# Performance work log

Measured on AMD Instinct MI355X. Metric: run time of the kernel, lower is better.

## Reference

```python
import jax, jax.numpy as jnp
import numpy as np

B, L, D = 2, 2048, 2048
H, KV = 32, 8
HD = D // H          # 64
REP = H // KV        # 4


def setup_inputs() -> dict:
    key = jax.random.key(0)
    ks = jax.random.split(key, 6)
    x = jax.random.normal(ks[0], (B, L, D), dtype=jnp.float32)
    # weights stored [in, out] (transpose of torch Linear weight), scaled for stability
    wq = jax.random.normal(ks[1], (D, H * HD), dtype=jnp.float32) * 0.02
    wk = jax.random.normal(ks[2], (D, KV * HD), dtype=jnp.float32) * 0.02
    wv = jax.random.normal(ks[3], (D, KV * HD), dtype=jnp.float32) * 0.02
    wo = jax.random.normal(ks[4], (H * HD, D), dtype=jnp.float32) * 0.02
    # RoPE frequencies: freqs_cis = exp(i * pos * theta), theta_j = 10000^{-2j/HD}
    inv_freq = 1.0 / (10000.0 ** (jnp.arange(0, HD, 2, dtype=jnp.float32) / HD))  # [HD/2]
    angles = jnp.arange(L, dtype=jnp.float32)[:, None] * inv_freq[None, :]        # [L, HD/2]
    freqs_cos = jnp.cos(angles)
    freqs_sin = jnp.sin(angles)
    # additive causal mask [L, L] (prefill from start_pos=0)
    mask = jnp.where(jnp.tril(jnp.ones((L, L), dtype=bool)), 0.0, -jnp.inf).astype(jnp.float32)
    return {"x": x, "start_pos": 0, "freqs_cos": freqs_cos, "freqs_sin": freqs_sin,
            "mask": mask, "wq": wq, "wk": wk, "wv": wv, "wo": wo}


def _apply_rope(t, cos, sin):
    # t: [B, L, h, HD]; cos/sin: [L, HD/2] -> broadcast [1, L, 1, HD/2]
    tp = t.reshape(*t.shape[:-1], HD // 2, 2)
    a, b = tp[..., 0], tp[..., 1]
    c = cos[None, :, None, :]
    s = sin[None, :, None, :]
    ra = a * c - b * s
    rb = a * s + b * c
    return jnp.stack([ra, rb], axis=-1).reshape(t.shape)


def reference(x, start_pos, freqs_cos, freqs_sin, mask, wq, wk, wv, wo):
    xq = jnp.einsum('bld,de->ble', x, wq).reshape(B, L, H, HD)
    xk = jnp.einsum('bld,de->ble', x, wk).reshape(B, L, KV, HD)
    xv = jnp.einsum('bld,de->ble', x, wv).reshape(B, L, KV, HD)
    xq = _apply_rope(xq, freqs_cos, freqs_sin)
    xk = _apply_rope(xk, freqs_cos, freqs_sin)
    # (cache write of xk/xv is a dead side effect in the torch module; omitted)
    # GQA: query head (g*REP + r) attends to kv head g  == repeat_interleave semantics
    q = xq.transpose(0, 2, 1, 3).reshape(B, KV, REP, L, HD)  # [B,KV,REP,L,HD]
    k = xk.transpose(0, 2, 1, 3)                              # [B,KV,L,HD]
    v = xv.transpose(0, 2, 1, 3)
    scale = 1.0 / jnp.sqrt(jnp.float32(HD))
    scores = jnp.einsum('bgrld,bgmd->bgrlm', q, k) * scale + mask  # [B,KV,REP,L,L]
    attn = jax.nn.softmax(scores, axis=-1)
    out = jnp.einsum('bgrlm,bgmd->bgrld', attn, v)            # [B,KV,REP,L,HD]
    out = out.reshape(B, H, L, HD).transpose(0, 2, 1, 3).reshape(B, L, H * HD)
    return jnp.einsum('ble,ed->bld', out, wo)
```

## Files before the change

kernel.cpp:

```cpp
#include <hip/hip_runtime.h>
#include <hip/hip_bf16.h>
#include <math.h>

typedef __bf16 bf16_t;
typedef __bf16 bf16x8 __attribute__((ext_vector_type(8)));
typedef __bf16 bf16x4 __attribute__((ext_vector_type(4)));
typedef __bf16 bf16x2 __attribute__((ext_vector_type(2)));
typedef float  f32x4  __attribute__((ext_vector_type(4)));
typedef int    i32x4  __attribute__((ext_vector_type(4)));

#define B_  2
#define L_  2048
#define D_  2048
#define H_  32
#define KV_ 8
#define HD_ 64

static __device__ __forceinline__ void gload_lds16(const bf16_t* g, void* l)
{
    __builtin_amdgcn_global_load_lds(
        (const __attribute__((address_space(1))) void*)g,
        (__attribute__((address_space(3))) void*)l, 16, 0, 0);
}

static __device__ __forceinline__ int packbf(float a, float b)
{
    bf16x2 t; t[0] = (bf16_t)a; t[1] = (bf16_t)b;
    return __builtin_bit_cast(int, t);
}

static __device__ __forceinline__ void pl32(int& a, int& b)
{
    asm("v_permlane32_swap_b32 %0, %1" : "+v"(a), "+v"(b));
}
static __device__ __forceinline__ void pl16(int& a, int& b)
{
    asm("v_permlane16_swap_b32 %0, %1" : "+v"(a), "+v"(b));
}

#define WAITV3() asm volatile("s_waitcnt vmcnt(3)" ::: "memory")
#define WAITV2() asm volatile("s_waitcnt vmcnt(2)" ::: "memory")
#define WAITV0() asm volatile("s_waitcnt vmcnt(0)" ::: "memory")
#define WAITL0() asm volatile("s_waitcnt lgkmcnt(0)" ::: "memory")

__global__ void prep_k(const float* __restrict__ wq, const float* __restrict__ wk,
                       const float* __restrict__ wv, const float* __restrict__ wo,
                       const float* __restrict__ xf,
                       bf16_t* __restrict__ Wqkv, bf16_t* __restrict__ WoT,
                       bf16_t* __restrict__ xb)
{
    __shared__ bf16_t tile[32][33];
    const int z  = blockIdx.z;
    const int tx = threadIdx.x, ty = threadIdx.y;

    if (z == 4) {
        const size_t base = ((size_t)(blockIdx.y * 64 + blockIdx.x) * 256
                             + ty * 32 + tx) * 8;
        const float4 v0 = *(const float4*)(xf + base);
        const float4 v1 = *(const float4*)(xf + base + 4);
        bf16x8 o;
        o[0] = (bf16_t)v0.x; o[1] = (bf16_t)v0.y; o[2] = (bf16_t)v0.z; o[3] = (bf16_t)v0.w;
        o[4] = (bf16_t)v1.x; o[5] = (bf16_t)v1.y; o[6] = (bf16_t)v1.z; o[7] = (bf16_t)v1.w;
        *(bf16x8*)(xb + base) = o;
        return;
    }

    const float* in; bf16_t* out; int C;
    if (z == 0)      { in = wq; out = Wqkv;                  C = 2048; }
    else if (z == 1) { in = wk; out = Wqkv + 2048ull * 2048; C = 512;  }
    else if (z == 2) { in = wv; out = Wqkv + 2560ull * 2048; C = 512;  }
    else             { in = wo; out = WoT;                   C = 2048; }

    const int bx = blockIdx.x * 32, by = blockIdx.y * 32;
    if (bx >= C) return;
    const int R = 2048;
#pragma unroll
    for (int i = ty; i < 32; i += 8)
        tile[i][tx] = (bf16_t)in[(size_t)(by + i) * C + bx + tx];
    __syncthreads();
#pragma unroll
    for (int i = ty; i < 32; i += 8)
        out[(size_t)(bx + i) * R + by + tx] = tile[tx][i];
}

template <typename InT>
__global__ void transpose_cast(const InT* __restrict__ in, bf16_t* __restrict__ out,
                               int R, int C)
{
    __shared__ bf16_t tile[32][33];
    const int bx = blockIdx.x * 32, by = blockIdx.y * 32;
    in  += (size_t)blockIdx.z * R * C;
    out += (size_t)blockIdx.z * R * C;
    const int tx = threadIdx.x, ty = threadIdx.y;
#pragma unroll
    for (int i = ty; i < 32; i += 8)
        tile[i][tx] = (bf16_t)(float)in[(size_t)(by + i) * C + bx + tx];
    __syncthreads();
#pragma unroll
    for (int i = ty; i < 32; i += 8)
        out[(size_t)(bx + i) * R + by + tx] = tile[tx][i];
}

#define FRAG(base, row, kk) \
    (*(const bf16x8*)((base) + (size_t)(row) * 128 + ((((kk) * 4 + quad) ^ sw8) << 4)))

#define STG_A(kt, h, buf) do {                                                        \
    gload_lds16(Ag + (size_t)((h) * 128)      * 2048 + (size_t)(kt) * 64,             \
                sdst + (buf) * 32768 + (h) * 16384);                                  \
    gload_lds16(Ag + (size_t)((h) * 128 + 64) * 2048 + (size_t)(kt) * 64,             \
                sdst + (buf) * 32768 + (h) * 16384 + 8192);                           \
} while (0)

#define STG_BU(kt, u, buf)                                                            \
    gload_lds16(Bg + (size_t)((u) * 64) * 2048 + (size_t)(kt) * 64,                   \
                sdst + 65536 + (buf) * 24576 + (u) * 8192)

#define QTILE(AB, BB, S1, S2, S3, S4, VMW)                                            \
  {                                  \
    _Pragma("unroll") for (int m = 0; m < 4; m++) {                                   \
        Afr[m][0] = FRAG(AB, arow + m * 16, 0);                                       \
        Afr[m][1] = FRAG(AB, arow + m * 16, 1); }                                     \
    _Pragma("unroll") for (int n = 0; n < 2; n++) {                                   \
        B01[n][0] = FRAG(BB, brow + n * 16, 0);                                       \
        B01[n][1] = FRAG(BB, brow + n * 16, 1); }                                     \
    S1;                                                                               \
    asm volatile("s_waitcnt lgkmcnt(8)" ::: "memory");                                \
    __builtin_amdgcn_s_barrier();                                                     \
    WAITL0();                                                                         \
    __builtin_amdgcn_s_setprio(1);                                                    \
    _Pragma("unroll") for (int m = 0; m < 4; m++)                                     \
      _Pragma("unroll") for (int n = 0; n < 2; n++)                                   \
        _Pragma("unroll") for (int kk = 0; kk < 2; kk++)                              \
          acc[m][n] = __builtin_amdgcn_mfma_f32_16x16x32_bf16(                        \
              Afr[m][kk], B01[n][kk], acc[m][n], 0, 0, 0);                            \
    __builtin_amdgcn_s_setprio(0);                                                    \
    __builtin_amdgcn_s_barrier();                                                     \
  }                                                                                   \
  {                                              \
    B2f[0] = FRAG(BB, brow + 32, 0);                                                  \
    B2f[1] = FRAG(BB, brow + 32, 1);                                                  \
    S2;                                                                               \
    __builtin_amdgcn_s_barrier();                                                     \
    WAITL0();                                                                         \
    __builtin_amdgcn_s_setprio(1);                                                    \
    _Pragma("unroll") for (int m = 0; m < 4; m++)                                     \
      _Pragma("unroll") for (int kk = 0; kk < 2; kk++)                                \
          acc[m][2] = __builtin_amdgcn_mfma_f32_16x16x32_bf16(                        \
              Afr[m][kk], B2f[kk], acc[m][2], 0, 0, 0);                               \
    __builtin_amdgcn_s_setprio(0);                                                    \
    __builtin_amdgcn_s_barrier();                                                     \
  }                                                                                   \
  {                                            \
    _Pragma("unroll") for (int m = 0; m < 4; m++) {                                   \
        Afr[m][0] = FRAG(AB, arow + (m + 4) * 16, 0);                                 \
        Afr[m][1] = FRAG(AB, arow + (m + 4) * 16, 1); }                               \
    S3;                                                                               \
    __builtin_amdgcn_s_barrier();                                                     \
    WAITL0();                                                                         \
    __builtin_amdgcn_s_setprio(1);                                                    \
    _Pragma("unroll") for (int m = 0; m < 4; m++)                                     \
      _Pragma("unroll") for (int kk = 0; kk < 2; kk++)                                \
          acc[m + 4][2] = __builtin_amdgcn_mfma_f32_16x16x32_bf16(                    \
              Afr[m][kk], B2f[kk], acc[m + 4][2], 0, 0, 0);                           \
    __builtin_amdgcn_s_setprio(0);                                                    \
    __builtin_amdgcn_s_barrier();                                                     \
  }                                                                                   \
  {                                \
    S4;                                                                               \
    VMW;                                                                              \
    __builtin_amdgcn_s_barrier();                                                     \
    __builtin_amdgcn_s_setprio(1);                                                    \
    _Pragma("unroll") for (int m = 0; m < 4; m++)                                     \
      _Pragma("unroll") for (int n = 0; n < 2; n++)                                   \
        _Pragma("unroll") for (int kk = 0; kk < 2; kk++)                              \
          acc[m + 4][n] = __builtin_amdgcn_mfma_f32_16x16x32_bf16(                    \
              Afr[m][kk], B01[n][kk], acc[m + 4][n], 0, 0, 0);                        \
    __builtin_amdgcn_s_setprio(0);                                                    \
    __builtin_amdgcn_s_barrier();                                                     \
  }

__global__ __launch_bounds__(512, 2) void gemm_qkv(
    const bf16_t* __restrict__ A,
    const bf16_t* __restrict__ BT,
    bf16_t* __restrict__ Qb, bf16_t* __restrict__ Kb, bf16_t* __restrict__ Vb)
{
    extern __shared__ __attribute__((aligned(16))) char DLDS[];
    constexpr int NITER = 2048 / 64 / 2;

    const int tid  = threadIdx.x;
    const int wave = tid >> 6;
    const int lane = tid & 63;
    const int quad = lane >> 4;
    const int l16  = lane & 15;
    const int wr   = wave >> 2;
    const int wc   = wave & 3;

    const int id   = blockIdx.x;
    const int w    = id >> 3;
    const int m0   = ((id & 7) * 2 + (w & 1)) * 256;
    const int n0   = (w >> 1) * 192;

    const int srow  = tid >> 3;
    const int swcol = ((tid & 7) ^ (srow & 7)) * 8;
    const bf16_t* Ag = A  + (size_t)(m0 + srow) * 2048 + swcol;
    const bf16_t* Bg = BT + (size_t)(n0 + srow) * 2048 + swcol;
    char* sdst = DLDS + tid * 16;

    const char* AB0 = DLDS;
    const char* AB1 = DLDS + 32768;
    const char* BB0 = DLDS + 65536;
    const char* BB1 = DLDS + 90112;
    const int sw8  = l16 & 7;
    const int arow = wr * 128 + l16;
    const int brow = wc * 48 + l16;

    f32x4 acc[8][3];
    const f32x4 zf = {0.f, 0.f, 0.f, 0.f};
#pragma unroll
    for (int i = 0; i < 8; i++)
#pragma unroll
        for (int j = 0; j < 3; j++) acc[i][j] = zf;

    bf16x8 Afr[4][2], B01[2][2], B2f[2];

    STG_BU(0, 0, 0); STG_BU(0, 1, 0); STG_BU(0, 2, 0);
    STG_A(0, 0, 0);  STG_A(0, 1, 0);
    STG_BU(1, 0, 1); STG_BU(1, 1, 1); STG_BU(1, 2, 1);
    WAITV3();
    __builtin_amdgcn_s_barrier();

    for (int i = 0; i < NITER; ++i) {
        const int t1 = 2 * i + 1;
        const int t2 = 2 * i + 2;
        const int t3 = 2 * i + 3;
        const bool more = (i + 1 < NITER);

        QTILE(AB0, BB0,
              STG_A(t1, 0, 1),
              STG_A(t1, 1, 1),
              if (more) { STG_BU(t2, 0, 0); STG_BU(t2, 1, 0); },
              if (more) { STG_BU(t2, 2, 0); },
              if (more) { WAITV3(); } else { WAITV0(); })
        QTILE(AB1, BB1,
              if (more) STG_A(t2, 0, 0),
              if (more) STG_A(t2, 1, 0),
              if (more) { STG_BU(t3, 0, 1); STG_BU(t3, 1, 1); },
              if (more) { STG_BU(t3, 2, 1); },
              if (more) { WAITV3(); } else { WAITV0(); })
    }

    const float cs = 0.18033688011112042f;
#pragma unroll
    for (int mt = 0; mt < 8; mt++)
#pragma unroll
        for (int nt = 0; nt < 3; nt++)
#pragma unroll
            for (int r = 0; r < 4; r++) {
                const int row  = m0 + wr * 128 + mt * 16 + quad * 4 + r;
                const int gcol = n0 + wc * 48 + nt * 16 + l16;
                const float v  = acc[mt][nt][r];
                if (gcol < 2048)
                    Qb[(size_t)row * 2048 + gcol] = (bf16_t)v;
                else if (gcol < 2560)
                    Kb[(size_t)row * 512 + (gcol - 2048)] = (bf16_t)(v * cs);
                else
                    Vb[(size_t)row * 512 + (gcol - 2560)] = (bf16_t)v;
            }
}

#undef FRAG
#undef STG_A
#undef STG_BU
#undef QTILE

#define OFRAG(base, row, kk) \
    (*(const bf16x8*)((base) + (size_t)(row) * 128 + ((((kk) * 4 + quad) ^ sw8) << 4)))

#define OSTG_A(kt, h, buf) do {                                                       \
    gload_lds16(Ag + (size_t)((h) * 128)      * 2048 + (size_t)(kt) * 64,             \
                adst + (buf) * 32768 + (h) * 16384);                                  \
    gload_lds16(Ag + (size_t)((h) * 128 + 64) * 2048 + (size_t)(kt) * 64,             \
                adst + (buf) * 32768 + (h) * 16384 + 8192);                           \
} while (0)

#define OSTG_B(kt, buf) do {                                                          \
    gload_lds16(Bg + (size_t)(kt) * 64,                       bdst + (buf) * 16384);  \
    gload_lds16(Bg + (size_t)64 * 2048 + (size_t)(kt) * 64,   bdst + (buf) * 16384 + 8192); \
} while (0)

#define OTILE(AB, BB, SA, SB, VMW)                                                    \
  {                                             \
    _Pragma("unroll") for (int m = 0; m < 4; m++) {                                   \
        Afr[m][0] = OFRAG(AB, arow + m * 16, 0);                                      \
        Afr[m][1] = OFRAG(AB, arow + m * 16, 1); }                                    \
    _Pragma("unroll") for (int n = 0; n < 2; n++) {                                   \
        Bfr[n][0] = OFRAG(BB, brow + n * 16, 0);                                      \
        Bfr[n][1] = OFRAG(BB, brow + n * 16, 1); }                                    \
    SA;                                                                               \
    asm volatile("s_waitcnt lgkmcnt(8)" ::: "memory");                                \
    __builtin_amdgcn_s_barrier();                                                     \
    WAITL0();                                                                         \
    __builtin_amdgcn_s_setprio(1);                                                    \
    _Pragma("unroll") for (int m = 0; m < 4; m++)                                     \
      _Pragma("unroll") for (int n = 0; n < 2; n++)                                   \
        _Pragma("unroll") for (int kk = 0; kk < 2; kk++)                              \
          acc[m][n] = __builtin_amdgcn_mfma_f32_16x16x32_bf16(                        \
              Afr[m][kk], Bfr[n][kk], acc[m][n], 0, 0, 0);                            \
    __builtin_amdgcn_s_setprio(0);                                                    \
    __builtin_amdgcn_s_barrier();                                                     \
  }                                                                                   \
  {                                \
    _Pragma("unroll") for (int m = 0; m < 4; m++) {                                   \
        Afr[m][0] = OFRAG(AB, arow + (m + 4) * 16, 0);                                \
        Afr[m][1] = OFRAG(AB, arow + (m + 4) * 16, 1); }                              \
    SB;                                                                               \
    VMW;                                                                              \
    __builtin_amdgcn_s_barrier();                                                     \
    WAITL0();                                                                         \
    __builtin_amdgcn_s_setprio(1);                                                    \
    _Pragma("unroll") for (int m = 0; m < 4; m++)                                     \
      _Pragma("unroll") for (int n = 0; n < 2; n++)                                   \
        _Pragma("unroll") for (int kk = 0; kk < 2; kk++)                              \
          acc[m + 4][n] = __builtin_amdgcn_mfma_f32_16x16x32_bf16(                    \
              Afr[m][kk], Bfr[n][kk], acc[m + 4][n], 0, 0, 0);                        \
    __builtin_amdgcn_s_setprio(0);                                                    \
    __builtin_amdgcn_s_barrier();                                                     \
  }

__global__ __launch_bounds__(512, 2) void gemm_out(
    const bf16_t* __restrict__ A,
    const bf16_t* __restrict__ BT,
    float* __restrict__ C)
{
    extern __shared__ __attribute__((aligned(16))) char DLDS[];
    constexpr int NITER = 2048 / 64 / 2;

    const int tid  = threadIdx.x;
    const int wave = tid >> 6;
    const int lane = tid & 63;
    const int quad = lane >> 4;
    const int l16  = lane & 15;
    const int wr   = wave >> 2;
    const int wc   = wave & 3;

    const int id   = blockIdx.x;
    const int w    = id >> 3;
    const int m0   = ((id & 7) * 2 + (w & 1)) * 256;
    const int n0   = (w >> 1) * 128;

    const int srow  = tid >> 3;
    const int swcol = ((tid & 7) ^ (srow & 7)) * 8;
    const bf16_t* Ag = A  + (size_t)(m0 + srow) * 2048 + swcol;
    const bf16_t* Bg = BT + (size_t)(n0 + srow) * 2048 + swcol;
    char* adst = DLDS + tid * 16;
    char* bdst = DLDS + 65536 + tid * 16;

    const char* AB0 = DLDS;
    const char* AB1 = DLDS + 32768;
    const char* BB0 = DLDS + 65536;
    const char* BB1 = DLDS + 81920;
    const int sw8  = l16 & 7;
    const int arow = wr * 128 + l16;
    const int brow = wc * 32 + l16;

    f32x4 acc[8][2];
    const f32x4 zf = {0.f, 0.f, 0.f, 0.f};
#pragma unroll
    for (int i = 0; i < 8; i++)
#pragma unroll
        for (int j = 0; j < 2; j++) acc[i][j] = zf;

    bf16x8 Afr[4][2], Bfr[2][2];

    OSTG_B(0, 0); OSTG_A(0, 0, 0); OSTG_A(0, 1, 0); OSTG_B(1, 1);
    WAITV2();
    __builtin_amdgcn_s_barrier();

    for (int i = 0; i < NITER; ++i) {
        const int v  = 2 * i + 1;
        const int t2 = 2 * i + 2;
        const int t3 = 2 * i + 3;
        const bool more = (i + 1 < NITER);

        OTILE(AB0, BB0,
              { OSTG_A(v, 0, 1); OSTG_A(v, 1, 1); },
              { if (more) OSTG_B(t2, 0); },
              if (more) { WAITV2(); } else { WAITV0(); })
        OTILE(AB1, BB1,
              { if (more) { OSTG_A(t2, 0, 0); OSTG_A(t2, 1, 0); } },
              { if (more) OSTG_B(t3, 1); },
              if (more) { WAITV2(); } else { WAITV0(); })
    }

#pragma unroll
    for (int mt = 0; mt < 8; mt++)
#pragma unroll
        for (int nt = 0; nt < 2; nt++)
#pragma unroll
            for (int r = 0; r < 4; r++) {
                const int row = m0 + wr * 128 + mt * 16 + quad * 4 + r;
                const int col = n0 + wc * 32 + nt * 16 + l16;
                C[(size_t)row * 2048 + col] = acc[mt][nt][r];
            }
}

#undef OFRAG
#undef OSTG_A
#undef OSTG_B
#undef OTILE

__global__ void rope2_k(bf16_t* __restrict__ Qb, bf16_t* __restrict__ Kb,
                        const float* __restrict__ fc, const float* __restrict__ fs)
{
    int idx = blockIdx.x * 256 + threadIdx.x;
    bf16_t* T; int nheads;
    if (idx < B_ * L_ * 32 * 8) { T = Qb; nheads = 32; }
    else { T = Kb; nheads = 8; idx -= B_ * L_ * 32 * 8; }

    const int g  = idx & 7;
    const int t  = idx >> 3;
    const int h  = t % nheads;
    const int bl = t / nheads;
    const int l  = bl & (L_ - 1);
    const float4 c4 = *(const float4*)(fc + l * 32 + g * 4);
    const float4 s4 = *(const float4*)(fs + l * 32 + g * 4);
    const size_t off = ((size_t)bl * nheads + h) * 64 + g * 8;
    const bf16x8 v = *(const bf16x8*)(T + off);
    const float cc[4] = {c4.x, c4.y, c4.z, c4.w};
    const float ss[4] = {s4.x, s4.y, s4.z, s4.w};
    bf16x8 o;
#pragma unroll
    for (int p = 0; p < 4; p++) {
        const float a  = (float)v[2 * p];
        const float b2 = (float)v[2 * p + 1];
        o[2 * p]     = (bf16_t)(a * cc[p] - b2 * ss[p]);
        o[2 * p + 1] = (bf16_t)(a * ss[p] + b2 * cc[p]);
    }
    *(bf16x8*)(T + off) = o;
}

__global__ __launch_bounds__(256, 2) void attn_k(
    const bf16_t* __restrict__ Q,
    const bf16_t* __restrict__ Kc,
    const bf16_t* __restrict__ VT,
    bf16_t* __restrict__ Ob)
{
    __shared__ __attribute__((aligned(16))) char LDS[32768];
    float* OL = (float*)LDS;
    float* LR = (float*)(LDS + 17408);

    const int tid  = threadIdx.x;
    const int wave = tid >> 6;
    const int lane = tid & 63;
    const int quad = lane >> 4;
    const int l16  = lane & 15;

    const int id   = blockIdx.y * 16 + blockIdx.x;
    const int c    = (id >> 3) & 15;
    const int bh   = (id & 7) * 8 + (id >> 7);
    const int bb   = bh >> 5;
    const int h    = bh & 31;
    const int kvh  = h >> 2;
    const size_t bbL = (size_t)bb * L_;

    const int schunk = ((lane & 3) ^ ((lane >> 3) & 3)) * 8;
    const int sw16   = ((l16 >> 1) & 3) * 16;

    const bf16_t* Kg = Kc + bbL * (KV_ * HD_) + kvh * HD_;
    const bf16_t* Vg = VT + (size_t)(bb * KV_ + kvh) * HD_ * L_;
    const bf16_t* KgL = Kg + (size_t)(wave * 32 + (lane >> 2)) * (KV_ * HD_) + schunk;
    const bf16_t* VgL = Vg + (size_t)(lane >> 2) * L_ + wave * 32 + schunk;
    char* kdst0 = (char*)LDS + wave * 2048 + (lane << 4);
    char* vdst0 = (char*)LDS + 16384 + wave * 4096 + (lane << 4);

    const f32x4 zf = {0.f, 0.f, 0.f, 0.f};

    for (int half = 0; half < 2; ++half) {
        const int j     = half ? c : 31 - c;
        const int qbase = j * 64;
        const int nkt   = (j + 2) >> 1;

        bf16x8 qf[4][2];
#pragma unroll
        for (int qt = 0; qt < 4; qt++) {
            const bf16_t* qrow = Q + ((bbL + qbase + qt * 16 + l16) * H_ + h) * HD_;
            qf[qt][0] = *(const bf16x8*)(qrow + quad * 8);
            qf[qt][1] = *(const bf16x8*)(qrow + 32 + quad * 8);
        }

        f32x4 acc[4][4];
#pragma unroll
        for (int mt = 0; mt < 4; mt++)
#pragma unroll
            for (int qt = 0; qt < 4; qt++) acc[mt][qt] = zf;
        float lacc[4] = {0.f, 0.f, 0.f, 0.f};

#pragma unroll
        for (int cc = 0; cc < 2; cc++)
#pragma unroll
            for (int sub = 0; sub < 2; sub++)
                gload_lds16(KgL + (size_t)(sub * 16) * (KV_ * HD_) + cc * 32,
                            kdst0 + cc * 8192 + sub * 1024);
#pragma unroll
        for (int sub = 0; sub < 4; sub++)
            gload_lds16(VgL + (size_t)(sub * 16) * L_, vdst0 + sub * 1024);

        for (int kt = 0; kt < nkt; kt++) {
            WAITV0();

            const char* Kld = LDS;
            const char* Vld = LDS + 16384;

            bf16x8 kf[2][2];
#pragma unroll
            for (int t = 0; t < 2; t++)
#pragma unroll
                for (int cc = 0; cc < 2; cc++)
                    kf[t][cc] = *(const bf16x8*)(Kld + cc * 8192 +
                        (wave * 32 + t * 16 + l16) * 64 + ((quad * 16) ^ sw16));

            bf16x8 vf[4];
#pragma unroll
            for (int mt = 0; mt < 4; mt++)
                vf[mt] = *(const bf16x8*)(Vld + wave * 4096 +
                    (mt * 16 + l16) * 64 + ((quad * 16) ^ sw16));

            WAITL0();

            if (kt + 1 < nkt) {
                const int ktb = (kt + 1) * 128;
#pragma unroll
                for (int cc = 0; cc < 2; cc++)
#pragma unroll
                    for (int sub = 0; sub < 2; sub++)
                        gload_lds16(KgL + (size_t)(ktb + sub * 16) * (KV_ * HD_) + cc * 32,
                                    kdst0 + cc * 8192 + sub * 1024);
#pragma unroll
                for (int sub = 0; sub < 4; sub++)
                    gload_lds16(VgL + (size_t)(sub * 16) * L_ + ktb,
                                vdst0 + sub * 1024);
            }

            f32x4 st[2][4];
            __builtin_amdgcn_s_setprio(1);
#pragma unroll
            for (int t = 0; t < 2; t++)
#pragma unroll
                for (int qt = 0; qt < 4; qt++) {
                    f32x4 s = __builtin_amdgcn_mfma_f32_16x16x32_bf16(
                        kf[t][0], qf[qt][0], zf, 0, 0, 0);
                    st[t][qt] = __builtin_amdgcn_mfma_f32_16x16x32_bf16(
                        kf[t][1], qf[qt][1], s, 0, 0, 0);
                }
            __builtin_amdgcn_s_setprio(0);

            if (kt == nkt - 1) {
                const int kq = kt * 128 + wave * 32 + quad * 4 - qbase - l16;
#pragma unroll
                for (int t = 0; t < 2; t++)
#pragma unroll
                    for (int qt = 0; qt < 4; qt++)
#pragma unroll
                        for (int r = 0; r < 4; r++)
                            st[t][qt][r] = (kq + t * 16 - qt * 16 + r <= 0)
                                         ? st[t][qt][r] : -__builtin_inff();
            }

            int pk[2][4][2];
#pragma unroll
            for (int t = 0; t < 2; t++)
#pragma unroll
                for (int qt = 0; qt < 4; qt++) {
                    const float e0 = __builtin_amdgcn_exp2f(st[t][qt][0]);
                    const float e1 = __builtin_amdgcn_exp2f(st[t][qt][1]);
                    const float e2 = __builtin_amdgcn_exp2f(st[t][qt][2]);
                    const float e3 = __builtin_amdgcn_exp2f(st[t][qt][3]);
                    lacc[qt] += (e0 + e1) + (e2 + e3);
                    pk[t][qt][0] = packbf(e0, e1);
                    pk[t][qt][1] = packbf(e2, e3);
                }

#pragma unroll
            for (int qt = 0; qt < 4; qt++) {
                int a0 = pk[0][qt][0], b0 = pk[1][qt][0];
                pl32(a0, b0); pl16(a0, b0);
                int a1 = pk[0][qt][1], b1 = pk[1][qt][1];
                pl32(a1, b1); pl16(a1, b1);
                i32x4 bi;
                bi[0] = a0; bi[1] = a1; bi[2] = b0; bi[3] = b1;
                const bf16x8 pb = __builtin_bit_cast(bf16x8, bi);
                __builtin_amdgcn_s_setprio(1);
#pragma unroll
                for (int mt = 0; mt < 4; mt++)
                    acc[mt][qt] = __builtin_amdgcn_mfma_f32_16x16x32_bf16(
                        vf[mt], pb, acc[mt][qt], 0, 0, 0);
                __builtin_amdgcn_s_setprio(0);
            }
        }

        float lw[4];
#pragma unroll
        for (int qt = 0; qt < 4; qt++) {
            float v = lacc[qt];
            v += __shfl_xor(v, 16);
            v += __shfl_xor(v, 32);
            lw[qt] = v;
        }

        __syncthreads();

        if (quad == 0)
#pragma unroll
            for (int qt = 0; qt < 4; qt++)
                LR[(wave * 4 + qt) * 16 + l16] = lw[qt];

#pragma unroll
        for (int p = 0; p < 4; p++) {
#pragma unroll
            for (int qt = 0; qt < 4; qt++) {
                if (((qt - wave) & 3) == p) {
#pragma unroll
                    for (int mt = 0; mt < 4; mt++) {
                        float* a = OL + (qt * 16 + l16) * 68 + mt * 16 + quad * 4;
                        if (p == 0) *(f32x4*)a = acc[mt][qt];
                        else        *(f32x4*)a = *(f32x4*)a + acc[mt][qt];
                    }
                }
            }
            __syncthreads();
        }

        const float ls = LR[(0 * 4 + wave) * 16 + l16] + LR[(1 * 4 + wave) * 16 + l16]
                       + LR[(2 * 4 + wave) * 16 + l16] + LR[(3 * 4 + wave) * 16 + l16];
        const float inv = 1.f / ls;
        bf16_t* orow = Ob + ((bbL + qbase + wave * 16 + l16) * H_ + h) * HD_;
#pragma unroll
        for (int j2 = 0; j2 < 4; j2++) {
            const f32x4 v = *(const f32x4*)(OL + (wave * 16 + l16) * 68 + quad * 16 + j2 * 4);
            bf16x4 o;
#pragma unroll
            for (int i = 0; i < 4; i++) o[i] = (bf16_t)(v[i] * inv);
            *(bf16x4*)(orow + quad * 16 + j2 * 4) = o;
        }
        __syncthreads();
    }
}

extern "C" void kernel_launch(void* const* d_in, const int* in_sizes, int n_in,
                              void* d_out, int out_size, void* d_ws, size_t ws_size,
                              hipStream_t stream)
{
    (void)in_sizes; (void)n_in; (void)out_size; (void)ws_size;
    const float* xf = (const float*)d_in[0];
    const float* fc = (const float*)d_in[2];
    const float* fs = (const float*)d_in[3];
    const float* wq = (const float*)d_in[5];
    const float* wk = (const float*)d_in[6];
    const float* wv = (const float*)d_in[7];
    const float* wo = (const float*)d_in[8];
    float* out = (float*)d_out;

    char* ws = (char*)d_ws;
    bf16_t* xb   = (bf16_t*)(ws);
    bf16_t* Qb   = (bf16_t*)(ws + (16ull << 20));
    bf16_t* Kb   = (bf16_t*)(ws + (32ull << 20));
    bf16_t* Vb   = (bf16_t*)(ws + (36ull << 20));
    bf16_t* VTb  = (bf16_t*)(ws + (40ull << 20));
    bf16_t* Oa   = (bf16_t*)(ws + (44ull << 20));
    bf16_t* Wqkv = (bf16_t*)(ws + (60ull << 20));
    bf16_t* WoT  = (bf16_t*)(ws + (72ull << 20));

    const dim3 tb(32, 8);
    prep_k<<<dim3(64, 64, 5), tb, 0, stream>>>(wq, wk, wv, wo, xf, Wqkv, WoT, xb);

    gemm_qkv<<<dim3(256), 512, 114688, stream>>>(xb, Wqkv, Qb, Kb, Vb);

    rope2_k<<<5120, 256, 0, stream>>>(Qb, Kb, fc, fs);

    transpose_cast<bf16_t><<<dim3(16, 64, 2), tb, 0, stream>>>(Vb, VTb, 2048, 512);

    attn_k<<<dim3(16, 64), 256, 0, stream>>>(Qb, Kb, VTb, Oa);

    gemm_out<<<dim3(256), 512, 98304, stream>>>(Oa, WoT, out);
}
```

Measured before the change: 296.6 us.

## Fuse rope and V transpose launches, compute softmax row sums via MFMA, raise attention occupancy

Merges the RoPE kernel and the V transpose kernel into one launch, using the z grid dimension to choose the work, which saves one kernel launch. In attention, the softmax denominator is now accumulated with an extra MFMA against a vector of ones instead of scalar adds followed by cross-lane shuffles. The attention kernel's launch bounds are raised from 2 to 4 blocks per CU, which limits register use and may cause spills. The row sum is now taken from the bf16-rounded probabilities rather than the fp32 values.

```diff
diff --git a/kernel.cpp b/kernel.cpp
--- a/kernel.cpp
+++ b/kernel.cpp
@@ -77,24 +77,6 @@
 #pragma unroll
     for (int i = ty; i < 32; i += 8)
         tile[i][tx] = (bf16_t)in[(size_t)(by + i) * C + bx + tx];
-    __syncthreads();
-#pragma unroll
-    for (int i = ty; i < 32; i += 8)
-        out[(size_t)(bx + i) * R + by + tx] = tile[tx][i];
-}
-
-template <typename InT>
-__global__ void transpose_cast(const InT* __restrict__ in, bf16_t* __restrict__ out,
-                               int R, int C)
-{
-    __shared__ bf16_t tile[32][33];
-    const int bx = blockIdx.x * 32, by = blockIdx.y * 32;
-    in  += (size_t)blockIdx.z * R * C;
-    out += (size_t)blockIdx.z * R * C;
-    const int tx = threadIdx.x, ty = threadIdx.y;
-#pragma unroll
-    for (int i = ty; i < 32; i += 8)
-        tile[i][tx] = (bf16_t)(float)in[(size_t)(by + i) * C + bx + tx];
     __syncthreads();
 #pragma unroll
     for (int i = ty; i < 32; i += 8)
@@ -409,10 +391,28 @@
 #undef OSTG_B
 #undef OTILE
 
-__global__ void rope2_k(bf16_t* __restrict__ Qb, bf16_t* __restrict__ Kb,
-                        const float* __restrict__ fc, const float* __restrict__ fs)
-{
-    int idx = blockIdx.x * 256 + threadIdx.x;
+__global__ void post_qkv_k(bf16_t* __restrict__ Qb, bf16_t* __restrict__ Kb,
+                           const bf16_t* __restrict__ Vb, bf16_t* __restrict__ VTb,
+                           const float* __restrict__ fc, const float* __restrict__ fs)
+{
+    const int z = blockIdx.z;
+    if (z < 2) {
+        __shared__ bf16_t tile[32][33];
+        const bf16_t* in = Vb + (size_t)z * 2048 * 512;
+        bf16_t* out = VTb + (size_t)z * 2048 * 512;
+        const int bx = blockIdx.x * 32, by = blockIdx.y * 32;
+        const int tx = threadIdx.x & 31, ty = threadIdx.x >> 5;
+#pragma unroll
+        for (int i = ty; i < 32; i += 8)
+            tile[i][tx] = in[(size_t)(by + i) * 512 + bx + tx];
+        __syncthreads();
+#pragma unroll
+        for (int i = ty; i < 32; i += 8)
+            out[(size_t)(bx + i) * 2048 + by + tx] = tile[tx][i];
+        return;
+    }
+
+    int idx = ((z - 2) * 1024 + blockIdx.y * 16 + blockIdx.x) * 256 + threadIdx.x;
     bf16_t* T; int nheads;
     if (idx < B_ * L_ * 32 * 8) { T = Qb; nheads = 32; }
     else { T = Kb; nheads = 8; idx -= B_ * L_ * 32 * 8; }
@@ -439,7 +439,7 @@
     *(bf16x8*)(T + off) = o;
 }
 
-__global__ __launch_bounds__(256, 2) void attn_k(
+__global__ __launch_bounds__(256, 4) void attn_k(
     const bf16_t* __restrict__ Q,
     const bf16_t* __restrict__ Kc,
     const bf16_t* __restrict__ VT,
@@ -474,6 +474,9 @@
     char* vdst0 = (char*)LDS + 16384 + wave * 4096 + (lane << 4);
 
     const f32x4 zf = {0.f, 0.f, 0.f, 0.f};
+    bf16x8 ones;
+#pragma unroll
+    for (int i = 0; i < 8; i++) ones[i] = (bf16_t)1.0f;
 
     for (int half = 0; half < 2; ++half) {
         const int j     = half ? c : 31 - c;
@@ -489,11 +492,13 @@
         }
 
         f32x4 acc[4][4];
+        f32x4 accl[4];
 #pragma unroll
         for (int mt = 0; mt < 4; mt++)
 #pragma unroll
             for (int qt = 0; qt < 4; qt++) acc[mt][qt] = zf;
-        float lacc[4] = {0.f, 0.f, 0.f, 0.f};
+#pragma unroll
+        for (int qt = 0; qt < 4; qt++) accl[qt] = zf;
 
 #pragma unroll
         for (int cc = 0; cc < 2; cc++)
@@ -575,7 +580,6 @@
                     const float e1 = __builtin_amdgcn_exp2f(st[t][qt][1]);
                     const float e2 = __builtin_amdgcn_exp2f(st[t][qt][2]);
                     const float e3 = __builtin_amdgcn_exp2f(st[t][qt][3]);
-                    lacc[qt] += (e0 + e1) + (e2 + e3);
                     pk[t][qt][0] = packbf(e0, e1);
                     pk[t][qt][1] = packbf(e2, e3);
                 }
@@ -594,25 +598,18 @@
                 for (int mt = 0; mt < 4; mt++)
                     acc[mt][qt] = __builtin_amdgcn_mfma_f32_16x16x32_bf16(
                         vf[mt], pb, acc[mt][qt], 0, 0, 0);
+                accl[qt] = __builtin_amdgcn_mfma_f32_16x16x32_bf16(
+                    ones, pb, accl[qt], 0, 0, 0);
                 __builtin_amdgcn_s_setprio(0);
             }
         }
 
-        float lw[4];
-#pragma unroll
-        for (int qt = 0; qt < 4; qt++) {
-            float v = lacc[qt];
-            v += __shfl_xor(v, 16);
-            v += __shfl_xor(v, 32);
-            lw[qt] = v;
-        }
-
         __syncthreads();
 
         if (quad == 0)
 #pragma unroll
             for (int qt = 0; qt < 4; qt++)
-                LR[(wave * 4 + qt) * 16 + l16] = lw[qt];
+                LR[(wave * 4 + qt) * 16 + l16] = accl[qt][0];
 
 #pragma unroll
         for (int p = 0; p < 4; p++) {
@@ -675,9 +672,7 @@
 
     gemm_qkv<<<dim3(256), 512, 114688, stream>>>(xb, Wqkv, Qb, Kb, Vb);
 
-    rope2_k<<<5120, 256, 0, stream>>>(Qb, Kb, fc, fs);
-
-    transpose_cast<bf16_t><<<dim3(16, 64, 2), tb, 0, stream>>>(Vb, VTb, 2048, 512);
+    post_qkv_k<<<dim3(16, 64, 7), 256, 0, stream>>>(Qb, Kb, Vb, VTb, fc, fs);
 
     attn_k<<<dim3(16, 64), 256, 0, stream>>>(Qb, Kb, VTb, Oa);
 
```

New measurement: 573.1 us. 1.93x slower.
